# Kernel tuning notes

Hardware: AMD Instinct MI355X
Metric: run time of the kernel (lower is better)

Reference implementation:

```python
import jax, jax.numpy as jnp
import numpy as np

LN_EPS = 1e-5


def setup_inputs() -> dict:
    key = jax.random.key(0)
    ks = jax.random.split(key, 7)
    b, n, dim_in = 2, 512, 256
    h, dim_out = 16, 128
    feats = jax.random.normal(ks[0], (b, n, dim_in), dtype=jnp.float32)
    ln_gamma = jnp.ones((dim_in,), dtype=jnp.float32)
    ln_beta = jnp.zeros((dim_in,), dtype=jnp.float32)
    # Linear weights stored as [in, out] so math is x @ W + b (same values as torch's x @ W_t.T)
    W_in = jax.random.normal(ks[1], (dim_in, 2 * h), dtype=jnp.float32) / np.sqrt(dim_in)
    b_in = jax.random.normal(ks[2], (2 * h,), dtype=jnp.float32) * 0.02
    W_out = jax.random.normal(ks[3], (dim_out, h * h), dtype=jnp.float32) / np.sqrt(h * h)
    b_out = jax.random.normal(ks[4], (dim_out,), dtype=jnp.float32) * 0.02
    return {"feats": feats, "ln_gamma": ln_gamma, "ln_beta": ln_beta,
            "W_in": W_in, "b_in": b_in, "W_out": W_out, "b_out": b_out}


def reference(feats, ln_gamma, ln_beta, W_in, b_in, W_out, b_out):
    # pre-norm (LayerNorm over last dim, eps=1e-5)
    mu = jnp.mean(feats, axis=-1, keepdims=True)
    var = jnp.mean(jnp.square(feats - mu), axis=-1, keepdims=True)
    x = (feats - mu) * jax.lax.rsqrt(var + LN_EPS) * ln_gamma + ln_beta
    # project_in then chunk into a [b,n,h] and bq [b,n,h]
    proj = x @ W_in + b_in
    h = proj.shape[-1] // 2
    a, bq = proj[..., :h], proj[..., h:]
    # outer product [b,n,m,p,q] -> reshape (p,q)->p*q, then project_out.
    # Fused: reshape W_out [d, h*h] -> [d, p, q] (row-major matches the reshape)
    Wd = W_out.reshape(W_out.shape[0], h, h)
    out = jnp.einsum('bnp,bmq,dpq->bnmd', a, bq, Wd) + b_out  # [b, n, n, dim_out]
    return out
```

## Files before the change

kernel.cpp:

```cpp
#include <hip/hip_runtime.h>

#define B 2
#define N 512
#define DIN 256
#define H 16
#define DOUT 128
#define ROWS (B * N)

typedef float f4 __attribute__((ext_vector_type(4)));

__global__ __launch_bounds__(256) void kA(const float* __restrict__ feats,
                                          const float* __restrict__ gamma,
                                          const float* __restrict__ beta,
                                          const float* __restrict__ Win,
                                          const float* __restrict__ bin,
                                          const float* __restrict__ Wout,
                                          float* __restrict__ bq_ws,
                                          float* __restrict__ T_ws) {
    const int row = blockIdx.x;
    const int t = threadIdx.x;

    __shared__ float sx[DIN];
    __shared__ float pp[256];
    __shared__ float pa[H];
    __shared__ float redA[4], redB[4];

    const float x = feats[row * DIN + t];

    float s = x;
#pragma unroll
    for (int o = 32; o; o >>= 1) s += __shfl_xor(s, o, 64);
    if ((t & 63) == 0) redA[t >> 6] = s;
    __syncthreads();
    const float mean = (redA[0] + redA[1] + redA[2] + redA[3]) * (1.0f / 256.0f);

    const float dx = x - mean;
    float s2 = dx * dx;
#pragma unroll
    for (int o = 32; o; o >>= 1) s2 += __shfl_xor(s2, o, 64);
    if ((t & 63) == 0) redB[t >> 6] = s2;
    __syncthreads();
    const float var = (redB[0] + redB[1] + redB[2] + redB[3]) * (1.0f / 256.0f);
    const float rstd = rsqrtf(var + 1e-5f);

    const float xn = dx * rstd * gamma[t] + beta[t];
    sx[t] = xn;
    __syncthreads();

    {
        const int k = t & 31;
        const int seg = t >> 5;
        const int j0 = seg * 32;
        float partial = 0.0f;
#pragma unroll
        for (int j = 0; j < 32; j++) {
            partial = fmaf(sx[j0 + j], Win[(j0 + j) * 32 + k], partial);
        }
        pp[t] = partial;
    }
    __syncthreads();

    if (t < 32) {
        float pr = bin[t];
#pragma unroll
        for (int h = 0; h < 8; h++) pr += pp[h * 32 + t];
        if (t < H) pa[t] = pr;
        else bq_ws[row * H + (t - H)] = pr;
    }
    __syncthreads();

    {
        const int d = t >> 1;
        const int q0 = (t & 1) * 8;
        float acc[8];
#pragma unroll
        for (int j = 0; j < 8; j++) acc[j] = 0.0f;
        const float* wp = Wout + d * 256 + q0;
#pragma unroll
        for (int p = 0; p < 16; p++) {
            const float av = pa[p];
            const float4* w4 = reinterpret_cast<const float4*>(wp + p * 16);
            const float4 w0 = w4[0], w1 = w4[1];
            acc[0] = fmaf(av, w0.x, acc[0]);
            acc[1] = fmaf(av, w0.y, acc[1]);
            acc[2] = fmaf(av, w0.z, acc[2]);
            acc[3] = fmaf(av, w0.w, acc[3]);
            acc[4] = fmaf(av, w1.x, acc[4]);
            acc[5] = fmaf(av, w1.y, acc[5]);
            acc[6] = fmaf(av, w1.z, acc[6]);
            acc[7] = fmaf(av, w1.w, acc[7]);
        }
        float4* dst = reinterpret_cast<float4*>(T_ws + row * (DOUT * H) + d * H + q0);
        dst[0] = make_float4(acc[0], acc[1], acc[2], acc[3]);
        dst[1] = make_float4(acc[4], acc[5], acc[6], acc[7]);
    }
}

__global__ __launch_bounds__(256) void kB(const float* __restrict__ bq_ws,
                                          const float* __restrict__ T_ws,
                                          const float* __restrict__ bout,
                                          float* __restrict__ out) {
    const int row = blockIdx.x;
    const int bb = row >> 9;
    const int t = threadIdx.x;
    const int d0 = (t & 31) * 4;
    const int ml = t >> 5;

    __shared__ float sbq[N * H];

    {
        const float4* src = reinterpret_cast<const float4*>(bq_ws + (size_t)bb * (N * H));
        float4* dst = reinterpret_cast<float4*>(sbq);
#pragma unroll
        for (int i = 0; i < 8; i++) dst[i * 256 + t] = src[i * 256 + t];
    }

    float Tr[4][16];
    const float4* Tv = reinterpret_cast<const float4*>(T_ws + (size_t)row * (DOUT * H));
#pragma unroll
    for (int i = 0; i < 4; i++) {
#pragma unroll
        for (int h = 0; h < 4; h++) {
            const float4 u = Tv[(d0 + i) * 4 + h];
            Tr[i][h * 4 + 0] = u.x;
            Tr[i][h * 4 + 1] = u.y;
            Tr[i][h * 4 + 2] = u.z;
            Tr[i][h * 4 + 3] = u.w;
        }
    }

    float bo[4];
#pragma unroll
    for (int i = 0; i < 4; i++) bo[i] = bout[d0 + i];

    __syncthreads();

    float* out_base = out + (size_t)row * (N * DOUT) + d0;

#pragma unroll 4
    for (int k = 0; k < 64; k++) {
        const int m = k * 8 + ml;
        const float4* bqv = reinterpret_cast<const float4*>(&sbq[m * H]);
        const float4 q0 = bqv[0], q1 = bqv[1], q2 = bqv[2], q3 = bqv[3];
        const float bv[16] = {q0.x, q0.y, q0.z, q0.w, q1.x, q1.y, q1.z, q1.w,
                              q2.x, q2.y, q2.z, q2.w, q3.x, q3.y, q3.z, q3.w};

        float acc[4] = {bo[0], bo[1], bo[2], bo[3]};
#pragma unroll
        for (int q = 0; q < 16; q++) {
#pragma unroll
            for (int i = 0; i < 4; i++) acc[i] = fmaf(bv[q], Tr[i][q], acc[i]);
        }

        f4 val = {acc[0], acc[1], acc[2], acc[3]};
        f4* dst = reinterpret_cast<f4*>(out_base + (size_t)m * DOUT);
        __builtin_nontemporal_store(val, dst);
    }
}

extern "C" void kernel_launch(void* const* d_in, const int* in_sizes, int n_in,
                              void* d_out, int out_size, void* d_ws, size_t ws_size,
                              hipStream_t stream) {
    const float* feats = (const float*)d_in[0];
    const float* gamma = (const float*)d_in[1];
    const float* beta  = (const float*)d_in[2];
    const float* Win   = (const float*)d_in[3];
    const float* bin   = (const float*)d_in[4];
    const float* Wout  = (const float*)d_in[5];
    const float* bout  = (const float*)d_in[6];

    float* bq_ws = (float*)d_ws;
    float* T_ws  = (float*)((char*)d_ws + 64 * 1024);

    kA<<<ROWS, 256, 0, stream>>>(feats, gamma, beta, Win, bin, Wout, bq_ws, T_ws);
    kB<<<ROWS, 256, 0, stream>>>(bq_ws, T_ws, bout, (float*)d_out);
}
```

Before: 296.9 us.

## Move T computation into output kernel and halve bq shared staging

The per-row T = a·Wout product now runs inside the output kernel and is kept in shared memory, so the 8 KB-per-row T workspace is no longer written to and read back from global memory. The bq tile is staged in two 256-row halves, which cuts shared memory per block and adds launch_bounds with a minimum of 4 blocks, aiming at higher occupancy. In exchange, every output block now reads Wout (128 KB, mostly from cache) and issues extra barriers. The kernel is dominated by the 256 MB output write, so any gain is likely small.

```diff
diff --git a/kernel.cpp b/kernel.cpp
--- a/kernel.cpp
+++ b/kernel.cpp
@@ -14,15 +14,13 @@
                                           const float* __restrict__ beta,
                                           const float* __restrict__ Win,
                                           const float* __restrict__ bin,
-                                          const float* __restrict__ Wout,
-                                          float* __restrict__ bq_ws,
-                                          float* __restrict__ T_ws) {
+                                          float* __restrict__ a_ws,
+                                          float* __restrict__ bq_ws) {
     const int row = blockIdx.x;
     const int t = threadIdx.x;
 
     __shared__ float sx[DIN];
     __shared__ float pp[256];
-    __shared__ float pa[H];
     __shared__ float redA[4], redB[4];
 
     const float x = feats[row * DIN + t];
@@ -64,10 +62,27 @@
         float pr = bin[t];
 #pragma unroll
         for (int h = 0; h < 8; h++) pr += pp[h * 32 + t];
-        if (t < H) pa[t] = pr;
+        if (t < H) a_ws[row * H + t] = pr;
         else bq_ws[row * H + (t - H)] = pr;
     }
-    __syncthreads();
+}
+
+__global__ __launch_bounds__(256, 4) void kB(const float* __restrict__ a_ws,
+                                             const float* __restrict__ bq_ws,
+                                             const float* __restrict__ Wout,
+                                             const float* __restrict__ bout,
+                                             float* __restrict__ out) {
+    const int row = blockIdx.x;
+    const int bb = row >> 9;
+    const int t = threadIdx.x;
+
+    __shared__ float Tt[H][DOUT];
+    __shared__ float sbq[256 * H];
+
+    const float* arow = a_ws + row * H;
+    float a_[H];
+#pragma unroll
+    for (int p = 0; p < H; p++) a_[p] = arow[p];
 
     {
         const int d = t >> 1;
@@ -77,8 +92,8 @@
         for (int j = 0; j < 8; j++) acc[j] = 0.0f;
         const float* wp = Wout + d * 256 + q0;
 #pragma unroll
-        for (int p = 0; p < 16; p++) {
-            const float av = pa[p];
+        for (int p = 0; p < H; p++) {
+            const float av = a_[p];
             const float4* w4 = reinterpret_cast<const float4*>(wp + p * 16);
             const float4 w0 = w4[0], w1 = w4[1];
             acc[0] = fmaf(av, w0.x, acc[0]);
@@ -90,71 +105,60 @@
             acc[6] = fmaf(av, w1.z, acc[6]);
             acc[7] = fmaf(av, w1.w, acc[7]);
         }
-        float4* dst = reinterpret_cast<float4*>(T_ws + row * (DOUT * H) + d * H + q0);
-        dst[0] = make_float4(acc[0], acc[1], acc[2], acc[3]);
-        dst[1] = make_float4(acc[4], acc[5], acc[6], acc[7]);
+#pragma unroll
+        for (int j = 0; j < 8; j++) Tt[q0 + j][d] = acc[j];
     }
-}
+    __syncthreads();
 
-__global__ __launch_bounds__(256) void kB(const float* __restrict__ bq_ws,
-                                          const float* __restrict__ T_ws,
-                                          const float* __restrict__ bout,
-                                          float* __restrict__ out) {
-    const int row = blockIdx.x;
-    const int bb = row >> 9;
-    const int t = threadIdx.x;
     const int d0 = (t & 31) * 4;
     const int ml = t >> 5;
-
-    __shared__ float sbq[N * H];
-
-    {
-        const float4* src = reinterpret_cast<const float4*>(bq_ws + (size_t)bb * (N * H));
-        float4* dst = reinterpret_cast<float4*>(sbq);
+    float Tr[4][16];
 #pragma unroll
-        for (int i = 0; i < 8; i++) dst[i * 256 + t] = src[i * 256 + t];
-    }
-
-    float Tr[4][16];
-    const float4* Tv = reinterpret_cast<const float4*>(T_ws + (size_t)row * (DOUT * H));
-#pragma unroll
-    for (int i = 0; i < 4; i++) {
-#pragma unroll
-        for (int h = 0; h < 4; h++) {
-            const float4 u = Tv[(d0 + i) * 4 + h];
-            Tr[i][h * 4 + 0] = u.x;
-            Tr[i][h * 4 + 1] = u.y;
-            Tr[i][h * 4 + 2] = u.z;
-            Tr[i][h * 4 + 3] = u.w;
-        }
+    for (int q = 0; q < H; q++) {
+        const float4 u = *reinterpret_cast<const float4*>(&Tt[q][d0]);
+        Tr[0][q] = u.x;
+        Tr[1][q] = u.y;
+        Tr[2][q] = u.z;
+        Tr[3][q] = u.w;
     }
 
     float bo[4];
 #pragma unroll
     for (int i = 0; i < 4; i++) bo[i] = bout[d0 + i];
 
-    __syncthreads();
-
+    const float* bq_base = bq_ws + (size_t)bb * (N * H);
     float* out_base = out + (size_t)row * (N * DOUT) + d0;
 
+#pragma unroll
+    for (int half = 0; half < 2; half++) {
+        __syncthreads();
+        {
+            const float4* src = reinterpret_cast<const float4*>(bq_base + half * (256 * H));
+            float4* dst = reinterpret_cast<float4*>(sbq);
+#pragma unroll
+            for (int i = 0; i < 4; i++) dst[i * 256 + t] = src[i * 256 + t];
+        }
+        __syncthreads();
+
 #pragma unroll 4
-    for (int k = 0; k < 64; k++) {
-        const int m = k * 8 + ml;
-        const float4* bqv = reinterpret_cast<const float4*>(&sbq[m * H]);
-        const float4 q0 = bqv[0], q1 = bqv[1], q2 = bqv[2], q3 = bqv[3];
-        const float bv[16] = {q0.x, q0.y, q0.z, q0.w, q1.x, q1.y, q1.z, q1.w,
-                              q2.x, q2.y, q2.z, q2.w, q3.x, q3.y, q3.z, q3.w};
+        for (int k = 0; k < 32; k++) {
+            const int ml_ = k * 8 + ml;
+            const float4* bqv = reinterpret_cast<const float4*>(&sbq[ml_ * H]);
+            const float4 q0 = bqv[0], q1 = bqv[1], q2 = bqv[2], q3 = bqv[3];
+            const float bv[16] = {q0.x, q0.y, q0.z, q0.w, q1.x, q1.y, q1.z, q1.w,
+                                  q2.x, q2.y, q2.z, q2.w, q3.x, q3.y, q3.z, q3.w};
 
-        float acc[4] = {bo[0], bo[1], bo[2], bo[3]};
+            float acc[4] = {bo[0], bo[1], bo[2], bo[3]};
 #pragma unroll
-        for (int q = 0; q < 16; q++) {
+            for (int q = 0; q < H; q++) {
 #pragma unroll
-            for (int i = 0; i < 4; i++) acc[i] = fmaf(bv[q], Tr[i][q], acc[i]);
+                for (int i = 0; i < 4; i++) acc[i] = fmaf(bv[q], Tr[i][q], acc[i]);
+            }
+
+            f4 val = {acc[0], acc[1], acc[2], acc[3]};
+            f4* dst = reinterpret_cast<f4*>(out_base + (size_t)(half * 256 + ml_) * DOUT);
+            __builtin_nontemporal_store(val, dst);
         }
-
-        f4 val = {acc[0], acc[1], acc[2], acc[3]};
-        f4* dst = reinterpret_cast<f4*>(out_base + (size_t)m * DOUT);
-        __builtin_nontemporal_store(val, dst);
     }
 }
 
@@ -169,9 +173,9 @@
     const float* Wout  = (const float*)d_in[5];
     const float* bout  = (const float*)d_in[6];
 
-    float* bq_ws = (float*)d_ws;
-    float* T_ws  = (float*)((char*)d_ws + 64 * 1024);
+    float* a_ws  = (float*)d_ws;
+    float* bq_ws = (float*)((char*)d_ws + 64 * 1024);
 
-    kA<<<ROWS, 256, 0, stream>>>(feats, gamma, beta, Win, bin, Wout, bq_ws, T_ws);
-    kB<<<ROWS, 256, 0, stream>>>(bq_ws, T_ws, bout, (float*)d_out);
+    kA<<<ROWS, 256, 0, stream>>>(feats, gamma, beta, Win, bin, a_ws, bq_ws);
+    kB<<<ROWS, 256, 0, stream>>>(a_ws, bq_ws, Wout, bout, (float*)d_out);
 }
```

Result: faster. 288.1 us (-2.9%).
